# Kernel optimization log

Measured on AMD Instinct MI355X. Metric: run time of the kernel, lower is better.

Reference implementation:

```python
import jax, jax.numpy as jnp
import numpy as np

SIGMA = 2.0
INF = 1.0e6


def setup_inputs() -> dict:
    key = jax.random.key(0)
    ks = jax.random.split(key, 6)
    M, N, H, C_IN, C_OUT, K = 50000, 50000, 32, 128, 128, 15
    q_pts = jax.random.normal(ks[0], (M, 3), dtype=jnp.float32)
    s_pts = jax.random.normal(ks[1], (N, 3), dtype=jnp.float32)
    s_feats = jax.random.normal(ks[2], (N, C_IN), dtype=jnp.float32)
    neighb_inds = jax.random.randint(ks[3], (M, H), 0, N)
    weights = jax.random.normal(ks[4], (K, C_IN, C_OUT), dtype=jnp.float32) * 0.05
    kernel_points = jax.random.normal(ks[5], (K, 3), dtype=jnp.float32)
    return {"q_pts": q_pts, "s_pts": s_pts, "s_feats": s_feats,
            "neighb_inds": neighb_inds, "weights": weights,
            "kernel_points": kernel_points}


def reference(q_pts, s_pts, s_feats, neighb_inds, weights, kernel_points):
    # Pad support points with a far-away shadow point and features with zeros
    s_pts_pad = jnp.concatenate([s_pts, jnp.full((1, s_pts.shape[1]), INF, s_pts.dtype)], axis=0)
    feats_pad = jnp.concatenate([s_feats, jnp.zeros((1, s_feats.shape[1]), s_feats.dtype)], axis=0)

    # Gather neighbors: (M, H, 3) relative positions, (M, H, C) features
    neighbors = s_pts_pad[neighb_inds] - q_pts[:, None, :]
    neighbor_feats = feats_pad[neighb_inds]

    # Kernel point influences (linear): (M, H, K)
    sq_dists = jnp.sum((neighbors[:, :, None, :] - kernel_points[None, None, :, :]) ** 2, axis=-1)
    influence = jnp.clip(1.0 - jnp.sqrt(sq_dists) / SIGMA, 0.0, None)

    # Aggregate neighbor features per kernel point: (M, K, C_in)
    weighted_feats = jnp.einsum('mhk,mhc->mkc', influence, neighbor_feats)

    # Per-kernel-point matmul summed over K (groups=1): (M, C_out)
    out = jnp.einsum('mkc,kcd->md', weighted_feats, weights)
    return out
```

## Files before the change

kernel.cpp:

```cpp
#include <hip/hip_runtime.h>
#include <cmath>


constexpr int HN = 32;
constexpr int KP = 15;
constexpr int CI = 128;
constexpr int CO = 128;
constexpr int MB = 32;
constexpr int NT = 1024;
constexpr float INV_SIGMA = 0.5f;

using short8 = __attribute__((ext_vector_type(8))) short;
using f32x4  = __attribute__((ext_vector_type(4))) float;

static __device__ __forceinline__ unsigned short f2bf(float x) {
    unsigned u = __float_as_uint(x);
    u += 0x7fff + ((u >> 16) & 1);
    return (unsigned short)(u >> 16);
}
static __device__ __forceinline__ float bf2f(unsigned short h) {
    return __uint_as_float(((unsigned)h) << 16);
}

__global__ void kpconv_prep_w(const float* __restrict__ w,
                              unsigned short* __restrict__ ws16) {
    int t = blockIdx.x * blockDim.x + threadIdx.x;
    int fb = t >> 6, lane = t & 63;
    if (fb >= 480) return;
    int k = fb >> 5, s = (fb >> 3) & 3, dt = fb & 7;
    int g = lane >> 4, n = lane & 15;
    unsigned short* base = ws16 + fb * 1024 + lane * 8;
    #pragma unroll
    for (int j = 0; j < 8; ++j) {
        int c = s * 32 + g * 8 + j;
        int d = dt * 16 + n;
        float v = w[(k * CI + c) * CO + d];
        unsigned short hi = f2bf(v);
        unsigned short lo = f2bf(v - bf2f(hi));
        base[j]       = (short)hi;
        base[512 + j] = (short)lo;
    }
}

#define MFMA(a, b, c) c = __builtin_amdgcn_mfma_f32_16x16x32_bf16(a, b, c, 0, 0, 0)

__global__ __launch_bounds__(NT)
void kpconv_main(const float* __restrict__ q_pts,
                 const float* __restrict__ s_pts,
                 const float* __restrict__ s_feats,
                 const int*   __restrict__ nb,
                 const float* __restrict__ kpts,
                 const unsigned short* __restrict__ wfr,
                 float* __restrict__ out, int M)
{
    __shared__ __align__(16) char pool[65536];

    const int t    = threadIdx.x;
    const int lane = t & 63;
    const int wid  = t >> 6;
    const int g    = lane >> 4;
    const int kk   = lane & 15;
    const int m0   = blockIdx.x * MB;

    const float kx = kpts[kk * 3 + 0];
    const float ky = kpts[kk * 3 + 1];
    const float kz = kpts[kk * 3 + 2];

    f32x4 accA[2][8] = {};

    #pragma unroll
    for (int pi = 0; pi < 2; ++pi) {
        const int  gp    = m0 + wid * 2 + pi;
        const bool valid = (gp < M);
        const int  rr    = valid ? gp : 0;
        const float qx = q_pts[rr * 3 + 0];
        const float qy = q_pts[rr * 3 + 1];
        const float qz = q_pts[rr * 3 + 2];

        int idx[8];
        #pragma unroll
        for (int j = 0; j < 8; ++j) idx[j] = nb[rr * HN + g * 8 + j];

        short8 Ih, Il;
        #pragma unroll
        for (int j = 0; j < 8; ++j) {
            const float* sp = s_pts + idx[j] * 3;
            float rx = sp[0] - qx, ry = sp[1] - qy, rz = sp[2] - qz;
            float dx = rx - kx, dy = ry - ky, dz = rz - kz;
            float d2 = dx * dx + dy * dy + dz * dz;
            float v  = fmaxf(1.0f - sqrtf(d2) * INV_SIGMA, 0.0f);
            if (kk == 15 || !valid) v = 0.0f;
            unsigned short hi = f2bf(v);
            Ih[j] = (short)hi;
            Il[j] = (short)f2bf(v - bf2f(hi));
        }

        #pragma unroll
        for (int ct = 0; ct < 8; ++ct) {
            float f[8];
            #pragma unroll
            for (int j = 0; j < 8; ++j)
                f[j] = s_feats[idx[j] * CI + ct * 16 + kk];
            short8 Fh, Fl;
            #pragma unroll
            for (int j = 0; j < 8; ++j) {
                unsigned short hi = f2bf(f[j]);
                Fh[j] = (short)hi;
                Fl[j] = (short)f2bf(f[j] - bf2f(hi));
            }
            MFMA(Ih, Fh, accA[pi][ct]);
            MFMA(Ih, Fl, accA[pi][ct]);
            MFMA(Il, Fh, accA[pi][ct]);
        }
    }

    const int kq = wid >> 2;
    const int dh = wid & 3;
    f32x4 accB[2][2] = {};

    #pragma unroll
    for (int tr = 0; tr < 4; ++tr) {
        if (tr) __syncthreads();
        #pragma unroll
        for (int pi = 0; pi < 2; ++pi) {
            const int prow = wid * 2 + pi;
            char* rowbase = pool + g * 16384 + prow * 256;
            const int rowx = (prow & 7) << 4;
            #pragma unroll
            for (int ct = 0; ct < 8; ++ct) {
                float v = accA[pi][ct][tr];
                unsigned short hi = f2bf(v);
                unsigned short lo = f2bf(v - bf2f(hi));
                int c2  = (ct * 16 + kk) * 2;
                int off = (c2 ^ (g << 5)) ^ rowx;
                *(unsigned short*)(rowbase + off)        = hi;
                *(unsigned short*)(rowbase + 8192 + off) = lo;
            }
        }
        __syncthreads();
        const int k = 4 * kq + tr;
        if (k < KP) {
            #pragma unroll
            for (int sc = 0; sc < 4; ++sc) {
                short8 ah[2], al[2];
                #pragma unroll
                for (int mt = 0; mt < 2; ++mt) {
                    int row = mt * 16 + kk;
                    int c2  = sc * 64 + g * 16;
                    int off = (c2 ^ (kq << 5)) ^ ((row & 7) << 4);
                    const char* base = pool + kq * 16384 + row * 256 + off;
                    ah[mt] = *(const short8*)(base);
                    al[mt] = *(const short8*)(base + 8192);
                }
                const unsigned short* fb0 =
                    wfr + ((k * 4 + sc) * 8 + dh * 2) * 1024 + lane * 8;
                short8 bh0 = *(const short8*)(fb0);
                short8 bl0 = *(const short8*)(fb0 + 512);
                short8 bh1 = *(const short8*)(fb0 + 1024);
                short8 bl1 = *(const short8*)(fb0 + 1536);
                MFMA(ah[0], bh0, accB[0][0]);
                MFMA(ah[0], bl0, accB[0][0]);
                MFMA(al[0], bh0, accB[0][0]);
                MFMA(ah[0], bh1, accB[0][1]);
                MFMA(ah[0], bl1, accB[0][1]);
                MFMA(al[0], bh1, accB[0][1]);
                MFMA(ah[1], bh0, accB[1][0]);
                MFMA(ah[1], bl0, accB[1][0]);
                MFMA(al[1], bh0, accB[1][0]);
                MFMA(ah[1], bh1, accB[1][1]);
                MFMA(ah[1], bl1, accB[1][1]);
                MFMA(al[1], bh1, accB[1][1]);
            }
        }
    }

    __syncthreads();
    float* red = (float*)pool;
    #pragma unroll
    for (int mt = 0; mt < 2; ++mt) {
        #pragma unroll
        for (int dti = 0; dti < 2; ++dti) {
            #pragma unroll
            for (int q = 0; q < 4; ++q) {
                int row = mt * 16 + g * 4 + q;
                int col = (dh * 2 + dti) * 16 + kk;
                red[(kq * 32 + row) * 128 + col] = accB[mt][dti][q];
            }
        }
    }
    __syncthreads();
    {
        int op = t >> 5, od = t & 31;
        const float4* r4 = (const float4*)red;
        float4 s0 = r4[(0 * 32 + op) * 32 + od];
        float4 s1 = r4[(1 * 32 + op) * 32 + od];
        float4 s2 = r4[(2 * 32 + op) * 32 + od];
        float4 s3 = r4[(3 * 32 + op) * 32 + od];
        float4 rv;
        rv.x = s0.x + s1.x + s2.x + s3.x;
        rv.y = s0.y + s1.y + s2.y + s3.y;
        rv.z = s0.z + s1.z + s2.z + s3.z;
        rv.w = s0.w + s1.w + s2.w + s3.w;
        if (m0 + op < M)
            ((float4*)out)[(m0 + op) * (CO / 4) + od] = rv;
    }
}

extern "C" void kernel_launch(void* const* d_in, const int* in_sizes, int n_in,
                              void* d_out, int out_size, void* d_ws, size_t ws_size,
                              hipStream_t stream)
{
    const float* q_pts   = (const float*)d_in[0];
    const float* s_pts   = (const float*)d_in[1];
    const float* s_feats = (const float*)d_in[2];
    const int*   nb      = (const int*)d_in[3];
    const float* weights = (const float*)d_in[4];
    const float* kpts    = (const float*)d_in[5];
    float*       out     = (float*)d_out;
    unsigned short* wpak = (unsigned short*)d_ws;

    int M = in_sizes[0] / 3;

    hipLaunchKernelGGL(kpconv_prep_w, dim3(120), dim3(256), 0, stream, weights, wpak);

    int grid = (M + MB - 1) / MB;
    hipLaunchKernelGGL(kpconv_main, dim3(grid), dim3(NT), 0, stream,
                       q_pts, s_pts, s_feats, nb, kpts, wpak, out, M);
}
```

Before: 305.5 us.

## Prefetch gathered features and weight fragments, vectorize index loads and bf16 splitting

Loads the neighbour indices as int4 vectors and hoists the support-point loads ahead of the influence computation. The feature gather is double-buffered one channel tile ahead. The hi/lo bf16 split now uses paired conversion intrinsics, which may map to packed convert instructions. Weight fragments for the second GEMM are issued before the barrier and prefetched one sub-chunk ahead, so global memory latency can overlap the MFMA work, at the cost of higher register pressure in a kernel launched with 1024 threads.

```diff
diff --git a/kernel.cpp b/kernel.cpp
--- a/kernel.cpp
+++ b/kernel.cpp
@@ -1,4 +1,5 @@
 #include <hip/hip_runtime.h>
+#include <hip/hip_bf16.h>
 #include <cmath>
 
 
@@ -12,6 +13,7 @@
 
 using short8 = __attribute__((ext_vector_type(8))) short;
 using f32x4  = __attribute__((ext_vector_type(4))) float;
+using uint4v = __attribute__((ext_vector_type(4))) unsigned int;
 
 static __device__ __forceinline__ unsigned short f2bf(float x) {
     unsigned u = __float_as_uint(x);
@@ -20,6 +22,17 @@
 }
 static __device__ __forceinline__ float bf2f(unsigned short h) {
     return __uint_as_float(((unsigned)h) << 16);
+}
+
+struct HL2 { unsigned h, l; };
+static __device__ __forceinline__ HL2 split2(float a, float b) {
+    __hip_bfloat162 hh = __float22bfloat162_rn(make_float2(a, b));
+    float2 hf = __bfloat1622float2(hh);
+    __hip_bfloat162 ll = __float22bfloat162_rn(make_float2(a - hf.x, b - hf.y));
+    HL2 r;
+    __builtin_memcpy(&r.h, &hh, 4);
+    __builtin_memcpy(&r.l, &ll, 4);
+    return r;
 }
 
 __global__ void kpconv_prep_w(const float* __restrict__ w,
@@ -77,37 +90,57 @@
         const float qy = q_pts[rr * 3 + 1];
         const float qz = q_pts[rr * 3 + 2];
 
-        int idx[8];
-        #pragma unroll
-        for (int j = 0; j < 8; ++j) idx[j] = nb[rr * HN + g * 8 + j];
-
-        short8 Ih, Il;
+        int4 ia = *(const int4*)(nb + rr * HN + g * 8);
+        int4 ib = *(const int4*)(nb + rr * HN + g * 8 + 4);
+        int idx[8] = { ia.x, ia.y, ia.z, ia.w, ib.x, ib.y, ib.z, ib.w };
+
+        const float* bp[8];
+        #pragma unroll
+        for (int j = 0; j < 8; ++j) bp[j] = s_feats + idx[j] * CI + kk;
+
+        float sx[8], sy[8], sz[8];
         #pragma unroll
         for (int j = 0; j < 8; ++j) {
             const float* sp = s_pts + idx[j] * 3;
-            float rx = sp[0] - qx, ry = sp[1] - qy, rz = sp[2] - qz;
+            sx[j] = sp[0]; sy[j] = sp[1]; sz[j] = sp[2];
+        }
+
+        float vj[8];
+        #pragma unroll
+        for (int j = 0; j < 8; ++j) {
+            float rx = sx[j] - qx, ry = sy[j] - qy, rz = sz[j] - qz;
             float dx = rx - kx, dy = ry - ky, dz = rz - kz;
             float d2 = dx * dx + dy * dy + dz * dz;
             float v  = fmaxf(1.0f - sqrtf(d2) * INV_SIGMA, 0.0f);
-            if (kk == 15 || !valid) v = 0.0f;
-            unsigned short hi = f2bf(v);
-            Ih[j] = (short)hi;
-            Il[j] = (short)f2bf(v - bf2f(hi));
-        }
-
+            vj[j] = (kk == 15 || !valid) ? 0.0f : v;
+        }
+        uint4v ihv, ilv;
+        #pragma unroll
+        for (int d = 0; d < 4; ++d) {
+            HL2 r = split2(vj[2 * d], vj[2 * d + 1]);
+            ihv[d] = r.h; ilv[d] = r.l;
+        }
+        short8 Ih = __builtin_bit_cast(short8, ihv);
+        short8 Il = __builtin_bit_cast(short8, ilv);
+
+        float fb2[2][8];
+        #pragma unroll
+        for (int j = 0; j < 8; ++j) fb2[0][j] = bp[j][0];
         #pragma unroll
         for (int ct = 0; ct < 8; ++ct) {
-            float f[8];
-            #pragma unroll
-            for (int j = 0; j < 8; ++j)
-                f[j] = s_feats[idx[j] * CI + ct * 16 + kk];
-            short8 Fh, Fl;
-            #pragma unroll
-            for (int j = 0; j < 8; ++j) {
-                unsigned short hi = f2bf(f[j]);
-                Fh[j] = (short)hi;
-                Fl[j] = (short)f2bf(f[j] - bf2f(hi));
-            }
+            if (ct < 7) {
+                #pragma unroll
+                for (int j = 0; j < 8; ++j) fb2[(ct + 1) & 1][j] = bp[j][(ct + 1) * 16];
+            }
+            const float* f = fb2[ct & 1];
+            uint4v hv, lv;
+            #pragma unroll
+            for (int d = 0; d < 4; ++d) {
+                HL2 r = split2(f[2 * d], f[2 * d + 1]);
+                hv[d] = r.h; lv[d] = r.l;
+            }
+            short8 Fh = __builtin_bit_cast(short8, hv);
+            short8 Fl = __builtin_bit_cast(short8, lv);
             MFMA(Ih, Fh, accA[pi][ct]);
             MFMA(Ih, Fl, accA[pi][ct]);
             MFMA(Il, Fh, accA[pi][ct]);
@@ -127,21 +160,41 @@
             char* rowbase = pool + g * 16384 + prow * 256;
             const int rowx = (prow & 7) << 4;
             #pragma unroll
-            for (int ct = 0; ct < 8; ++ct) {
-                float v = accA[pi][ct][tr];
-                unsigned short hi = f2bf(v);
-                unsigned short lo = f2bf(v - bf2f(hi));
-                int c2  = (ct * 16 + kk) * 2;
-                int off = (c2 ^ (g << 5)) ^ rowx;
-                *(unsigned short*)(rowbase + off)        = hi;
-                *(unsigned short*)(rowbase + 8192 + off) = lo;
-            }
+            for (int cp = 0; cp < 4; ++cp) {
+                HL2 r = split2(accA[pi][2 * cp][tr], accA[pi][2 * cp + 1][tr]);
+                int c2a  = ((2 * cp) * 16 + kk) * 2;
+                int c2b  = ((2 * cp + 1) * 16 + kk) * 2;
+                int offa = (c2a ^ (g << 5)) ^ rowx;
+                int offb = (c2b ^ (g << 5)) ^ rowx;
+                *(unsigned short*)(rowbase + offa)        = (unsigned short)(r.h & 0xffffu);
+                *(unsigned short*)(rowbase + offb)        = (unsigned short)(r.h >> 16);
+                *(unsigned short*)(rowbase + 8192 + offa) = (unsigned short)(r.l & 0xffffu);
+                *(unsigned short*)(rowbase + 8192 + offb) = (unsigned short)(r.l >> 16);
+            }
+        }
+        const int  k  = 4 * kq + tr;
+        const bool kv = (k < KP);
+        short8 cbh0, cbl0, cbh1, cbl1;
+        if (kv) {
+            const unsigned short* fb0 = wfr + ((k * 4 + 0) * 8 + dh * 2) * 1024 + lane * 8;
+            cbh0 = *(const short8*)(fb0);
+            cbl0 = *(const short8*)(fb0 + 512);
+            cbh1 = *(const short8*)(fb0 + 1024);
+            cbl1 = *(const short8*)(fb0 + 1536);
         }
         __syncthreads();
-        const int k = 4 * kq + tr;
-        if (k < KP) {
+        if (kv) {
             #pragma unroll
             for (int sc = 0; sc < 4; ++sc) {
+                short8 nh0, nl0, nh1, nl1;
+                if (sc < 3) {
+                    const unsigned short* fbn =
+                        wfr + ((k * 4 + sc + 1) * 8 + dh * 2) * 1024 + lane * 8;
+                    nh0 = *(const short8*)(fbn);
+                    nl0 = *(const short8*)(fbn + 512);
+                    nh1 = *(const short8*)(fbn + 1024);
+                    nl1 = *(const short8*)(fbn + 1536);
+                }
                 short8 ah[2], al[2];
                 #pragma unroll
                 for (int mt = 0; mt < 2; ++mt) {
@@ -152,24 +205,19 @@
                     ah[mt] = *(const short8*)(base);
                     al[mt] = *(const short8*)(base + 8192);
                 }
-                const unsigned short* fb0 =
-                    wfr + ((k * 4 + sc) * 8 + dh * 2) * 1024 + lane * 8;
-                short8 bh0 = *(const short8*)(fb0);
-                short8 bl0 = *(const short8*)(fb0 + 512);
-                short8 bh1 = *(const short8*)(fb0 + 1024);
-                short8 bl1 = *(const short8*)(fb0 + 1536);
-                MFMA(ah[0], bh0, accB[0][0]);
-                MFMA(ah[0], bl0, accB[0][0]);
-                MFMA(al[0], bh0, accB[0][0]);
-                MFMA(ah[0], bh1, accB[0][1]);
-                MFMA(ah[0], bl1, accB[0][1]);
-                MFMA(al[0], bh1, accB[0][1]);
-                MFMA(ah[1], bh0, accB[1][0]);
-                MFMA(ah[1], bl0, accB[1][0]);
-                MFMA(al[1], bh0, accB[1][0]);
-                MFMA(ah[1], bh1, accB[1][1]);
-                MFMA(ah[1], bl1, accB[1][1]);
-                MFMA(al[1], bh1, accB[1][1]);
+                MFMA(ah[0], cbh0, accB[0][0]);
+                MFMA(ah[0], cbl0, accB[0][0]);
+                MFMA(al[0], cbh0, accB[0][0]);
+                MFMA(ah[0], cbh1, accB[0][1]);
+                MFMA(ah[0], cbl1, accB[0][1]);
+                MFMA(al[0], cbh1, accB[0][1]);
+                MFMA(ah[1], cbh0, accB[1][0]);
+                MFMA(ah[1], cbl0, accB[1][0]);
+                MFMA(al[1], cbh0, accB[1][0]);
+                MFMA(ah[1], cbh1, accB[1][1]);
+                MFMA(ah[1], cbl1, accB[1][1]);
+                MFMA(al[1], cbh1, accB[1][1]);
+                if (sc < 3) { cbh0 = nh0; cbl0 = nl0; cbh1 = nh1; cbl1 = nl1; }
             }
         }
     }
@@ -220,10 +268,9 @@
     unsigned short* wpak = (unsigned short*)d_ws;
 
     int M = in_sizes[0] / 3;
+    int grid = (M + MB - 1) / MB;
 
     hipLaunchKernelGGL(kpconv_prep_w, dim3(120), dim3(256), 0, stream, weights, wpak);
-
-    int grid = (M + MB - 1) / MB;
     hipLaunchKernelGGL(kpconv_main, dim3(grid), dim3(NT), 0, stream,
                        q_pts, s_pts, s_feats, nb, kpts, wpak, out, M);
 }
```

Result: slower. 320.0 us (+4.8%).
